# Optimization experiments

Hardware: AMD Instinct MI355X
Metric: run time of the kernel (lower is better)

Reference implementation:

```python
import jax, jax.numpy as jnp
import numpy as np

B, A, N, G, F = 16, 256, 64, 64, 128  # batch, atoms, neighbors, gaussians, filters
CUTOFF = 5.0


def ssp(x):
    # shifted softplus: ln(0.5*e^x + 0.5)
    return jax.nn.softplus(x) - jnp.log(2.0).astype(x.dtype)


def setup_inputs() -> dict:
    key = jax.random.key(0)
    ks = jax.random.split(key, 10)
    x = jax.random.normal(ks[0], (B, A, F), jnp.float32)
    r_ij = jax.random.uniform(ks[1], (B, A, N), jnp.float32) * 6.0  # some beyond cutoff
    f_ij = jax.random.uniform(ks[2], (B, A, N, G), jnp.float32)  # gaussian-expanded dists
    neighbors = jax.random.randint(ks[3], (B, A, N), 0, A)
    pairwise_mask = (jax.random.uniform(ks[4], (B, A, N)) < 0.9).astype(jnp.float32)
    s = lambda fan: 1.0 / np.sqrt(fan)
    fw1 = jax.random.normal(ks[5], (G, F), jnp.float32) * s(G)
    fb1 = jnp.zeros((F,), jnp.float32)
    fw2 = jax.random.normal(ks[6], (F, F), jnp.float32) * s(F)
    fb2 = jnp.zeros((F,), jnp.float32)
    w_in2f = jax.random.normal(ks[7], (F, F), jnp.float32) * s(F)
    w_f2out = jax.random.normal(ks[8], (F, F), jnp.float32) * s(F)
    b_f2out = jnp.zeros((F,), jnp.float32)
    return {"x": x, "r_ij": r_ij, "f_ij": f_ij, "neighbors": neighbors,
            "pairwise_mask": pairwise_mask, "fw1": fw1, "fb1": fb1, "fw2": fw2,
            "fb2": fb2, "w_in2f": w_in2f, "w_f2out": w_f2out, "b_f2out": b_f2out}


def reference(x, r_ij, f_ij, neighbors, pairwise_mask,
              fw1, fb1, fw2, fb2, w_in2f, w_f2out, b_f2out):
    # filter network: Dense(G->F, ssp) -> Dense(F->F)
    W = ssp(jnp.einsum('bang,gf->banf', f_ij, fw1) + fb1)
    W = jnp.einsum('banf,fh->banh', W, fw2) + fb2  # [B,A,N,F]
    # cosine cutoff
    C = 0.5 * (jnp.cos(r_ij * (jnp.pi / CUTOFF)) + 1.0)
    C = C * (r_ij < CUTOFF).astype(r_ij.dtype)
    W = W * C[..., None]
    # in2f (no bias), then gather neighbor features along atom axis
    y = jnp.einsum('bad,df->baf', x, w_in2f)  # [B,A,F]
    bidx = jnp.arange(y.shape[0])[:, None, None]
    y_nbh = y[bidx, neighbors]  # [B,A,N,F]
    # filter-weight multiply + masked sum aggregate over neighbor axis
    y = jnp.sum(y_nbh * W * pairwise_mask[..., None], axis=2)  # [B,A,F]
    # f2out with shifted-softplus activation
    return ssp(jnp.einsum('baf,fo->bao', y, w_f2out) + b_f2out)
```

## Files before the change

kernel.cpp:

```cpp
#include <hip/hip_runtime.h>
#include <hip/hip_bf16.h>
#include <math.h>

#define B_ 16
#define A_ 256
#define N_ 64
#define G_ 64
#define F_ 128

typedef __attribute__((ext_vector_type(8))) short short8;
typedef __attribute__((ext_vector_type(4))) float floatx4;

__device__ __forceinline__ float ssp(float x) {
    const float t = __expf(-fabsf(x));
    return fmaxf(x, 0.0f) + __logf(1.0f + t) - 0.69314718055994531f;
}
__device__ __forceinline__ short f2bf(float f) {
    union { __hip_bfloat16 h; short s; } u;
    u.h = __float2bfloat16(f);
    return u.s;
}
__device__ __forceinline__ float bf2f(unsigned short u) {
    union { unsigned int i; float f; } v;
    v.i = ((unsigned)u) << 16;
    return v.f;
}

__global__ __launch_bounds__(256) void prep_weights(
    const float* __restrict__ fw1, const float* __restrict__ fw2,
    const float* __restrict__ win, const float* __restrict__ wout,
    unsigned short* __restrict__ fw1B, unsigned short* __restrict__ fw2B,
    unsigned short* __restrict__ winB, unsigned short* __restrict__ woutB)
{
    const int idx = blockIdx.x * 256 + threadIdx.x;
    if (idx < 8192) {
        const int j  = idx & 7;
        const int l  = (idx >> 3) & 63;
        const int ks = (idx >> 9) & 1;
        const int tf = idx >> 10;
        const int g  = ks * 32 + (l >> 4) * 8 + j;
        const int f  = tf * 16 + (l & 15);
        fw1B[idx] = (unsigned short)f2bf(fw1[g * F_ + f]);
    } else {
        const int i2 = (idx - 8192) & 16383;
        const int sel = (idx - 8192) >> 14;
        const int j  = i2 & 7;
        const int l  = (i2 >> 3) & 63;
        const int ks = (i2 >> 9) & 3;
        const int tf = i2 >> 11;
        const int k  = ks * 32 + (l >> 4) * 8 + j;
        const int f  = tf * 16 + (l & 15);
        const float* src = (sel == 0) ? fw2 : (sel == 1) ? win : wout;
        unsigned short* dst = (sel == 0) ? fw2B : (sel == 1) ? winB : woutB;
        dst[i2] = (unsigned short)f2bf(src[k * F_ + f]);
    }
}

template<int MODE>
__global__ __launch_bounds__(256) void gemm128_kernel(
    const void* __restrict__ Ain, const unsigned short* __restrict__ WB,
    const float* __restrict__ bias, void* __restrict__ Cout)
{
    const int tid = threadIdx.x;
    const int w = tid >> 6, l = tid & 63, quad = l >> 4, c0 = l & 15;
    const int row = blockIdx.x * 64 + w * 16 + c0;

    short8 a[4];
    if (MODE == 0) {
        const float* A = (const float*)Ain + (size_t)row * F_ + quad * 8;
        #pragma unroll
        for (int ks = 0; ks < 4; ++ks) {
            const float4 v0 = *(const float4*)(A + ks * 32);
            const float4 v1 = *(const float4*)(A + ks * 32 + 4);
            short8 t;
            t[0] = f2bf(v0.x); t[1] = f2bf(v0.y);
            t[2] = f2bf(v0.z); t[3] = f2bf(v0.w);
            t[4] = f2bf(v1.x); t[5] = f2bf(v1.y);
            t[6] = f2bf(v1.z); t[7] = f2bf(v1.w);
            a[ks] = t;
        }
    } else {
        const unsigned short* A = (const unsigned short*)Ain
                                + (size_t)row * F_ + quad * 8;
        #pragma unroll
        for (int ks = 0; ks < 4; ++ks)
            a[ks] = *(const short8*)(A + ks * 32);
    }

    const short8* W8 = (const short8*)WB;
    floatx4 acc[8];
    #pragma unroll
    for (int tf = 0; tf < 8; ++tf) acc[tf] = (floatx4){0.f, 0.f, 0.f, 0.f};
    #pragma unroll
    for (int ks = 0; ks < 4; ++ks)
        #pragma unroll
        for (int tf = 0; tf < 8; ++tf)
            acc[tf] = __builtin_amdgcn_mfma_f32_16x16x32_bf16(
                a[ks], W8[(tf * 4 + ks) * 64 + l], acc[tf], 0, 0, 0);

    #pragma unroll
    for (int tf = 0; tf < 8; ++tf) {
        #pragma unroll
        for (int r = 0; r < 4; ++r) {
            const int ro = blockIdx.x * 64 + w * 16 + quad * 4 + r;
            const int co = tf * 16 + c0;
            if (MODE == 0)
                ((unsigned short*)Cout)[(size_t)ro * F_ + co] =
                    (unsigned short)f2bf(acc[tf][r]);
            else
                ((float*)Cout)[(size_t)ro * F_ + co] = ssp(acc[tf][r] + bias[co]);
        }
    }
}

__global__ __launch_bounds__(256) void cfconv_kernel(
    const float* __restrict__ r_ij, const float* __restrict__ f_ij,
    const int*   __restrict__ nbrs, const float* __restrict__ mask,
    const float* __restrict__ fb1,  const float* __restrict__ fb2,
    const unsigned short* __restrict__ ypre,
    const unsigned short* __restrict__ fw1B,
    const unsigned short* __restrict__ fw2B,
    unsigned short* __restrict__ y_agg)
{
    __shared__ short s_h1[N_ * F_];
    __shared__ float s_scale[N_];
    __shared__ int   s_nb[N_];
    __shared__ float s_red[4][F_];

    const int blk  = blockIdx.x;
    const int tid  = threadIdx.x;
    const int b    = blk >> 8;
    const int w    = tid >> 6;
    const int l    = tid & 63;
    const int quad = l >> 4;
    const int c0   = l & 15;

    if (l < 16) {
        const int n = w * 16 + l;
        const float r = r_ij[(size_t)blk * N_ + n];
        const float c = (r < 5.0f)
            ? 0.5f * (cosf(r * 0.62831853071795865f) + 1.0f)
            : 0.0f;
        s_scale[n] = c * mask[(size_t)blk * N_ + n];
        s_nb[n]    = nbrs[(size_t)blk * N_ + n];
    }

    const short8* fw1B8 = (const short8*)fw1B;
    const short8* fw2B8 = (const short8*)fw2B;

    short8 a1[2];
    {
        const float* base = f_ij + (size_t)blk * (N_ * G_)
                          + (size_t)(w * 16 + c0) * G_ + quad * 8;
        #pragma unroll
        for (int ks = 0; ks < 2; ++ks) {
            const float4 v0 = *(const float4*)(base + ks * 32);
            const float4 v1 = *(const float4*)(base + ks * 32 + 4);
            short8 a;
            a[0] = f2bf(v0.x); a[1] = f2bf(v0.y);
            a[2] = f2bf(v0.z); a[3] = f2bf(v0.w);
            a[4] = f2bf(v1.x); a[5] = f2bf(v1.y);
            a[6] = f2bf(v1.z); a[7] = f2bf(v1.w);
            a1[ks] = a;
        }
    }
    floatx4 acc1[8];
    #pragma unroll
    for (int tf = 0; tf < 8; ++tf) acc1[tf] = (floatx4){0.f, 0.f, 0.f, 0.f};
    #pragma unroll
    for (int ks = 0; ks < 2; ++ks)
        #pragma unroll
        for (int tf = 0; tf < 8; ++tf)
            acc1[tf] = __builtin_amdgcn_mfma_f32_16x16x32_bf16(
                a1[ks], fw1B8[(tf * 2 + ks) * 64 + l], acc1[tf], 0, 0, 0);

    #pragma unroll
    for (int tf = 0; tf < 8; ++tf) {
        const float bias  = fb1[tf * 16 + c0];
        const int   chunk = tf * 2 + (c0 >> 3);
        const int   o     = c0 & 7;
        #pragma unroll
        for (int r = 0; r < 4; ++r) {
            const int row_l = quad * 4 + r;
            const float v = ssp(acc1[tf][r] + bias);
            s_h1[(w * 16 + row_l) * F_ + ((chunk ^ row_l) * 8) + o] = f2bf(v);
        }
    }

    short8 a2[4];
    #pragma unroll
    for (int ks = 0; ks < 4; ++ks)
        a2[ks] = *(const short8*)&s_h1[(w * 16 + c0) * F_
                                       + (((ks * 4 + quad) ^ c0) * 8)];
    floatx4 acc2[8];
    #pragma unroll
    for (int tf = 0; tf < 8; ++tf) acc2[tf] = (floatx4){0.f, 0.f, 0.f, 0.f};
    #pragma unroll
    for (int ks = 0; ks < 4; ++ks)
        #pragma unroll
        for (int tf = 0; tf < 8; ++tf)
            acc2[tf] = __builtin_amdgcn_mfma_f32_16x16x32_bf16(
                a2[ks], fw2B8[(tf * 4 + ks) * 64 + l], acc2[tf], 0, 0, 0);

    float bias2[8];
    #pragma unroll
    for (int tf = 0; tf < 8; ++tf) bias2[tf] = fb2[tf * 16 + c0];

    float part[8];
    #pragma unroll
    for (int tf = 0; tf < 8; ++tf) part[tf] = 0.0f;
    #pragma unroll
    for (int r = 0; r < 4; ++r) {
        const int n = w * 16 + quad * 4 + r;
        const float sc = s_scale[n];
        if (sc != 0.0f) {
            const unsigned short* yrow =
                ypre + (size_t)(b * A_ + s_nb[n]) * F_ + c0;
            #pragma unroll
            for (int tf = 0; tf < 8; ++tf)
                part[tf] = fmaf((acc2[tf][r] + bias2[tf]) * sc,
                                bf2f(yrow[tf * 16]), part[tf]);
        }
    }

    #pragma unroll
    for (int tf = 0; tf < 8; ++tf) {
        part[tf] += __shfl_xor(part[tf], 16, 64);
        part[tf] += __shfl_xor(part[tf], 32, 64);
    }
    if (l < 16) {
        #pragma unroll
        for (int tf = 0; tf < 8; ++tf)
            s_red[w][tf * 16 + l] = part[tf];
    }
    __syncthreads();

    if (tid < F_) {
        const float v = s_red[0][tid] + s_red[1][tid]
                      + s_red[2][tid] + s_red[3][tid];
        y_agg[(size_t)blk * F_ + tid] = (unsigned short)f2bf(v);
    }
}

extern "C" void kernel_launch(void* const* d_in, const int* in_sizes, int n_in,
                              void* d_out, int out_size, void* d_ws, size_t ws_size,
                              hipStream_t stream) {
    const float* x        = (const float*)d_in[0];
    const float* r_ij     = (const float*)d_in[1];
    const float* f_ij     = (const float*)d_in[2];
    const int*   nbrs     = (const int*)  d_in[3];
    const float* mask     = (const float*)d_in[4];
    const float* fw1      = (const float*)d_in[5];
    const float* fb1      = (const float*)d_in[6];
    const float* fw2      = (const float*)d_in[7];
    const float* fb2      = (const float*)d_in[8];
    const float* w_in2f   = (const float*)d_in[9];
    const float* w_f2out  = (const float*)d_in[10];
    const float* b_f2out  = (const float*)d_in[11];
    float* out = (float*)d_out;

    unsigned short* ypre  = (unsigned short*)d_ws;
    unsigned short* fw1B  = ypre  + (size_t)B_ * A_ * F_;
    unsigned short* fw2B  = fw1B  + 8192;
    unsigned short* winB  = fw2B  + 16384;
    unsigned short* woutB = winB  + 16384;
    unsigned short* y_agg = woutB + 16384;

    prep_weights<<<(8192 + 3 * 16384) / 256, 256, 0, stream>>>(
        fw1, fw2, w_in2f, w_f2out, fw1B, fw2B, winB, woutB);
    gemm128_kernel<0><<<B_ * A_ / 64, 256, 0, stream>>>(x, winB, nullptr, ypre);
    cfconv_kernel<<<B_ * A_, 256, 0, stream>>>(
        r_ij, f_ij, nbrs, mask, fb1, fb2, ypre, fw1B, fw2B, y_agg);
    gemm128_kernel<1><<<B_ * A_ / 64, 256, 0, stream>>>(y_agg, woutB, b_f2out, out);
}
```

Measured before the change: 163.2 us.

## Fuse weight prep with in2f GEMM and f2out GEMM into cfconv kernel

Merges weight conversion and the in2f GEMM into one launch: each block transposes w_in2f into LDS itself, and extra blocks convert the remaining weights. The f2out GEMM plus ssp moves into the tail of cfconv, so y_agg no longer round-trips through global memory and the launch count drops from four to two. The neighbor-row gathers are now issued before the second MFMA to hide latency, the scale-zero skip branch is removed, and cosf becomes __cosf. The cost is per-block redundant weight transposes and a 16-row MFMA tile used for a single output row in the fused f2out step.

```diff
diff --git a/kernel.cpp b/kernel.cpp
--- a/kernel.cpp
+++ b/kernel.cpp
@@ -15,63 +15,81 @@
     const float t = __expf(-fabsf(x));
     return fmaxf(x, 0.0f) + __logf(1.0f + t) - 0.69314718055994531f;
 }
-__device__ __forceinline__ short f2bf(float f) {
-    union { __hip_bfloat16 h; short s; } u;
-    u.h = __float2bfloat16(f);
-    return u.s;
+__device__ __forceinline__ unsigned short f2bf(float f) {
+    union { float f; unsigned u; } v; v.f = f;
+    v.u += 0x7fffu + ((v.u >> 16) & 1u);
+    return (unsigned short)(v.u >> 16);
 }
 __device__ __forceinline__ float bf2f(unsigned short u) {
-    union { unsigned int i; float f; } v;
+    union { unsigned i; float f; } v;
     v.i = ((unsigned)u) << 16;
     return v.f;
 }
 
-__global__ __launch_bounds__(256) void prep_weights(
+__global__ __launch_bounds__(256) void k1_prep_in2f(
+    const float* __restrict__ x,   const float* __restrict__ win,
     const float* __restrict__ fw1, const float* __restrict__ fw2,
-    const float* __restrict__ win, const float* __restrict__ wout,
+    const float* __restrict__ wout,
+    unsigned short* __restrict__ ypre,
     unsigned short* __restrict__ fw1B, unsigned short* __restrict__ fw2B,
-    unsigned short* __restrict__ winB, unsigned short* __restrict__ woutB)
+    unsigned short* __restrict__ woutB)
 {
-    const int idx = blockIdx.x * 256 + threadIdx.x;
-    if (idx < 8192) {
-        const int j  = idx & 7;
-        const int l  = (idx >> 3) & 63;
-        const int ks = (idx >> 9) & 1;
-        const int tf = idx >> 10;
-        const int g  = ks * 32 + (l >> 4) * 8 + j;
-        const int f  = tf * 16 + (l & 15);
-        fw1B[idx] = (unsigned short)f2bf(fw1[g * F_ + f]);
-    } else {
-        const int i2 = (idx - 8192) & 16383;
-        const int sel = (idx - 8192) >> 14;
-        const int j  = i2 & 7;
-        const int l  = (i2 >> 3) & 63;
-        const int ks = (i2 >> 9) & 3;
-        const int tf = i2 >> 11;
-        const int k  = ks * 32 + (l >> 4) * 8 + j;
-        const int f  = tf * 16 + (l & 15);
-        const float* src = (sel == 0) ? fw2 : (sel == 1) ? win : wout;
-        unsigned short* dst = (sel == 0) ? fw2B : (sel == 1) ? winB : woutB;
-        dst[i2] = (unsigned short)f2bf(src[k * F_ + f]);
-    }
-}
-
-template<int MODE>
-__global__ __launch_bounds__(256) void gemm128_kernel(
-    const void* __restrict__ Ain, const unsigned short* __restrict__ WB,
-    const float* __restrict__ bias, void* __restrict__ Cout)
-{
+    const int bid = blockIdx.x;
     const int tid = threadIdx.x;
+
+    if (bid >= 256) {
+        int idx = (bid - 256) * 1024 + tid * 4;
+        #pragma unroll
+        for (int u = 0; u < 4; ++u, ++idx) {
+            if (idx < 8192) {
+                const int j  = idx & 7;
+                const int l  = (idx >> 3) & 63;
+                const int ks = (idx >> 9) & 1;
+                const int tf = idx >> 10;
+                const int g  = ks * 32 + (l >> 4) * 8 + j;
+                const int f  = tf * 16 + (l & 15);
+                fw1B[idx] = f2bf(fw1[g * F_ + f]);
+            } else {
+                const int i2 = (idx - 8192) & 16383;
+                const int sel = (idx - 8192) >> 14;
+                const int j  = i2 & 7;
+                const int l  = (i2 >> 3) & 63;
+                const int ks = (i2 >> 9) & 3;
+                const int tf = i2 >> 11;
+                const int k  = ks * 32 + (l >> 4) * 8 + j;
+                const int f  = tf * 16 + (l & 15);
+                if (sel == 0) fw2B[i2]  = f2bf(fw2[k * F_ + f]);
+                else          woutB[i2] = f2bf(wout[k * F_ + f]);
+            }
+        }
+        return;
+    }
+
+    __shared__ unsigned short s_wt[128 * 136];
+
+    const float4* win4 = (const float4*)win;
+    for (int i = tid; i < 4096; i += 256) {
+        const float4 v = win4[i];
+        const int e = i * 4;
+        const int k = e >> 7;
+        const int f = e & 127;
+        s_wt[(f + 0) * 136 + k] = f2bf(v.x);
+        s_wt[(f + 1) * 136 + k] = f2bf(v.y);
+        s_wt[(f + 2) * 136 + k] = f2bf(v.z);
+        s_wt[(f + 3) * 136 + k] = f2bf(v.w);
+    }
+    __syncthreads();
+
     const int w = tid >> 6, l = tid & 63, quad = l >> 4, c0 = l & 15;
-    const int row = blockIdx.x * 64 + w * 16 + c0;
+    const int row0 = bid * 16;
 
     short8 a[4];
-    if (MODE == 0) {
-        const float* A = (const float*)Ain + (size_t)row * F_ + quad * 8;
+    {
+        const float* base = x + (size_t)(row0 + c0) * F_ + quad * 8;
         #pragma unroll
         for (int ks = 0; ks < 4; ++ks) {
-            const float4 v0 = *(const float4*)(A + ks * 32);
-            const float4 v1 = *(const float4*)(A + ks * 32 + 4);
+            const float4 v0 = *(const float4*)(base + ks * 32);
+            const float4 v1 = *(const float4*)(base + ks * 32 + 4);
             short8 t;
             t[0] = f2bf(v0.x); t[1] = f2bf(v0.y);
             t[2] = f2bf(v0.z); t[3] = f2bf(v0.w);
@@ -79,37 +97,29 @@
             t[6] = f2bf(v1.z); t[7] = f2bf(v1.w);
             a[ks] = t;
         }
-    } else {
-        const unsigned short* A = (const unsigned short*)Ain
-                                + (size_t)row * F_ + quad * 8;
-        #pragma unroll
-        for (int ks = 0; ks < 4; ++ks)
-            a[ks] = *(const short8*)(A + ks * 32);
-    }
-
-    const short8* W8 = (const short8*)WB;
-    floatx4 acc[8];
-    #pragma unroll
-    for (int tf = 0; tf < 8; ++tf) acc[tf] = (floatx4){0.f, 0.f, 0.f, 0.f};
-    #pragma unroll
-    for (int ks = 0; ks < 4; ++ks)
-        #pragma unroll
-        for (int tf = 0; tf < 8; ++tf)
-            acc[tf] = __builtin_amdgcn_mfma_f32_16x16x32_bf16(
-                a[ks], W8[(tf * 4 + ks) * 64 + l], acc[tf], 0, 0, 0);
-
-    #pragma unroll
-    for (int tf = 0; tf < 8; ++tf) {
-        #pragma unroll
-        for (int r = 0; r < 4; ++r) {
-            const int ro = blockIdx.x * 64 + w * 16 + quad * 4 + r;
-            const int co = tf * 16 + c0;
-            if (MODE == 0)
-                ((unsigned short*)Cout)[(size_t)ro * F_ + co] =
-                    (unsigned short)f2bf(acc[tf][r]);
-            else
-                ((float*)Cout)[(size_t)ro * F_ + co] = ssp(acc[tf][r] + bias[co]);
-        }
+    }
+
+    floatx4 acc[2];
+    acc[0] = (floatx4){0.f,0.f,0.f,0.f};
+    acc[1] = (floatx4){0.f,0.f,0.f,0.f};
+    #pragma unroll
+    for (int t = 0; t < 2; ++t) {
+        const int tf = w * 2 + t;
+        #pragma unroll
+        for (int ks = 0; ks < 4; ++ks) {
+            const short8 bfrag = *(const short8*)
+                &s_wt[(tf * 16 + c0) * 136 + ks * 32 + quad * 8];
+            acc[t] = __builtin_amdgcn_mfma_f32_16x16x32_bf16(
+                a[ks], bfrag, acc[t], 0, 0, 0);
+        }
+    }
+    #pragma unroll
+    for (int t = 0; t < 2; ++t) {
+        const int tf = w * 2 + t;
+        #pragma unroll
+        for (int r = 0; r < 4; ++r)
+            ypre[(size_t)(row0 + quad * 4 + r) * F_ + tf * 16 + c0] =
+                f2bf(acc[t][r]);
     }
 }
 
@@ -120,12 +130,15 @@
     const unsigned short* __restrict__ ypre,
     const unsigned short* __restrict__ fw1B,
     const unsigned short* __restrict__ fw2B,
-    unsigned short* __restrict__ y_agg)
+    const unsigned short* __restrict__ woutB,
+    const float* __restrict__ bf2out,
+    float* __restrict__ out)
 {
     __shared__ short s_h1[N_ * F_];
     __shared__ float s_scale[N_];
     __shared__ int   s_nb[N_];
     __shared__ float s_red[4][F_];
+    __shared__ unsigned short s_yfb[F_];
 
     const int blk  = blockIdx.x;
     const int tid  = threadIdx.x;
@@ -139,14 +152,15 @@
         const int n = w * 16 + l;
         const float r = r_ij[(size_t)blk * N_ + n];
         const float c = (r < 5.0f)
-            ? 0.5f * (cosf(r * 0.62831853071795865f) + 1.0f)
+            ? 0.5f * (__cosf(r * 0.62831853071795865f) + 1.0f)
             : 0.0f;
         s_scale[n] = c * mask[(size_t)blk * N_ + n];
         s_nb[n]    = nbrs[(size_t)blk * N_ + n];
     }
 
-    const short8* fw1B8 = (const short8*)fw1B;
-    const short8* fw2B8 = (const short8*)fw2B;
+    const short8* fw1B8  = (const short8*)fw1B;
+    const short8* fw2B8  = (const short8*)fw2B;
+    const short8* woutB8 = (const short8*)woutB;
 
     short8 a1[2];
     {
@@ -166,7 +180,7 @@
     }
     floatx4 acc1[8];
     #pragma unroll
-    for (int tf = 0; tf < 8; ++tf) acc1[tf] = (floatx4){0.f, 0.f, 0.f, 0.f};
+    for (int tf = 0; tf < 8; ++tf) acc1[tf] = (floatx4){0.f,0.f,0.f,0.f};
     #pragma unroll
     for (int ks = 0; ks < 2; ++ks)
         #pragma unroll
@@ -183,7 +197,8 @@
         for (int r = 0; r < 4; ++r) {
             const int row_l = quad * 4 + r;
             const float v = ssp(acc1[tf][r] + bias);
-            s_h1[(w * 16 + row_l) * F_ + ((chunk ^ row_l) * 8) + o] = f2bf(v);
+            s_h1[(w * 16 + row_l) * F_ + ((chunk ^ row_l) * 8) + o] =
+                (short)f2bf(v);
         }
     }
 
@@ -192,9 +207,25 @@
     for (int ks = 0; ks < 4; ++ks)
         a2[ks] = *(const short8*)&s_h1[(w * 16 + c0) * F_
                                        + (((ks * 4 + quad) ^ c0) * 8)];
+
+    int   rowoff[4];
+    float scl[4];
+    #pragma unroll
+    for (int r = 0; r < 4; ++r) {
+        const int n = w * 16 + quad * 4 + r;
+        scl[r]    = s_scale[n];
+        rowoff[r] = (b * A_ + s_nb[n]) * F_;
+    }
+    unsigned short yv[4][8];
+    #pragma unroll
+    for (int r = 0; r < 4; ++r)
+        #pragma unroll
+        for (int tf = 0; tf < 8; ++tf)
+            yv[r][tf] = ypre[rowoff[r] + tf * 16 + c0];
+
     floatx4 acc2[8];
     #pragma unroll
-    for (int tf = 0; tf < 8; ++tf) acc2[tf] = (floatx4){0.f, 0.f, 0.f, 0.f};
+    for (int tf = 0; tf < 8; ++tf) acc2[tf] = (floatx4){0.f,0.f,0.f,0.f};
     #pragma unroll
     for (int ks = 0; ks < 4; ++ks)
         #pragma unroll
@@ -202,26 +233,15 @@
             acc2[tf] = __builtin_amdgcn_mfma_f32_16x16x32_bf16(
                 a2[ks], fw2B8[(tf * 4 + ks) * 64 + l], acc2[tf], 0, 0, 0);
 
-    float bias2[8];
-    #pragma unroll
-    for (int tf = 0; tf < 8; ++tf) bias2[tf] = fb2[tf * 16 + c0];
-
     float part[8];
     #pragma unroll
     for (int tf = 0; tf < 8; ++tf) part[tf] = 0.0f;
     #pragma unroll
-    for (int r = 0; r < 4; ++r) {
-        const int n = w * 16 + quad * 4 + r;
-        const float sc = s_scale[n];
-        if (sc != 0.0f) {
-            const unsigned short* yrow =
-                ypre + (size_t)(b * A_ + s_nb[n]) * F_ + c0;
-            #pragma unroll
-            for (int tf = 0; tf < 8; ++tf)
-                part[tf] = fmaf((acc2[tf][r] + bias2[tf]) * sc,
-                                bf2f(yrow[tf * 16]), part[tf]);
-        }
-    }
+    for (int r = 0; r < 4; ++r)
+        #pragma unroll
+        for (int tf = 0; tf < 8; ++tf)
+            part[tf] = fmaf((acc2[tf][r] + fb2[tf * 16 + c0]) * scl[r],
+                            bf2f(yv[r][tf]), part[tf]);
 
     #pragma unroll
     for (int tf = 0; tf < 8; ++tf) {
@@ -238,7 +258,32 @@
     if (tid < F_) {
         const float v = s_red[0][tid] + s_red[1][tid]
                       + s_red[2][tid] + s_red[3][tid];
-        y_agg[(size_t)blk * F_ + tid] = (unsigned short)f2bf(v);
+        s_yfb[tid] = f2bf(v);
+    }
+    __syncthreads();
+
+    short8 ya[4];
+    #pragma unroll
+    for (int ks = 0; ks < 4; ++ks)
+        ya[ks] = *(const short8*)&s_yfb[ks * 32 + quad * 8];
+
+    floatx4 aco[2];
+    aco[0] = (floatx4){0.f,0.f,0.f,0.f};
+    aco[1] = (floatx4){0.f,0.f,0.f,0.f};
+    #pragma unroll
+    for (int t = 0; t < 2; ++t) {
+        const int tf = w * 2 + t;
+        #pragma unroll
+        for (int ks = 0; ks < 4; ++ks)
+            aco[t] = __builtin_amdgcn_mfma_f32_16x16x32_bf16(
+                ya[ks], woutB8[(tf * 4 + ks) * 64 + l], aco[t], 0, 0, 0);
+    }
+    if (quad == 0) {
+        #pragma unroll
+        for (int t = 0; t < 2; ++t) {
+            const int c = (w * 2 + t) * 16 + c0;
+            out[(size_t)blk * F_ + c] = ssp(aco[t][0] + bf2out[c]);
+        }
     }
 }
 
@@ -262,14 +307,11 @@
     unsigned short* ypre  = (unsigned short*)d_ws;
     unsigned short* fw1B  = ypre  + (size_t)B_ * A_ * F_;
     unsigned short* fw2B  = fw1B  + 8192;
-    unsigned short* winB  = fw2B  + 16384;
-    unsigned short* woutB = winB  + 16384;
-    unsigned short* y_agg = woutB + 16384;
-
-    prep_weights<<<(8192 + 3 * 16384) / 256, 256, 0, stream>>>(
-        fw1, fw2, w_in2f, w_f2out, fw1B, fw2B, winB, woutB);
-    gemm128_kernel<0><<<B_ * A_ / 64, 256, 0, stream>>>(x, winB, nullptr, ypre);
+    unsigned short* woutB = fw2B  + 16384;
+
+    k1_prep_in2f<<<296, 256, 0, stream>>>(
+        x, w_in2f, fw1, fw2, w_f2out, ypre, fw1B, fw2B, woutB);
     cfconv_kernel<<<B_ * A_, 256, 0, stream>>>(
-        r_ij, f_ij, nbrs, mask, fb1, fb2, ypre, fw1B, fw2B, y_agg);
-    gemm128_kernel<1><<<B_ * A_ / 64, 256, 0, stream>>>(y_agg, woutB, b_f2out, out);
-}
+        r_ij, f_ij, nbrs, mask, fb1, fb2,
+        ypre, fw1B, fw2B, woutB, b_f2out, out);
+}
```

Result: slower. 166.8 us (+2.2%).
